# Optimization experiments

Measured on AMD Instinct MI355X. Metric: run time of the kernel, lower is better.

Reference implementation:

```python
import jax, jax.numpy as jnp
import numpy as np

# Mamba dims: d_model=1024, expand=2 -> d_inner=2048, d_state=16, d_conv=4, dt_rank=ceil(1024/16)=64
B, L, D = 2, 1024, 1024
DIN, N, R, K = 2048, 16, 64, 4
LN_EPS = 1e-5


def setup_inputs():
    key = jax.random.key(0)
    ks = jax.random.split(key, 12)
    s = lambda fan_in: 1.0 / np.sqrt(fan_in)
    inp = {
        "x": jax.random.normal(ks[0], (B, L, D), jnp.float32),
        "W_in": jax.random.normal(ks[1], (D, 2 * DIN), jnp.float32) * s(D),
        "conv_w": jax.random.normal(ks[2], (DIN, K), jnp.float32) * s(K),
        "conv_b": jax.random.normal(ks[3], (DIN,), jnp.float32) * 0.02,
        "W_x": jax.random.normal(ks[4], (DIN, R + 2 * N), jnp.float32) * s(DIN),
        "W_dt": jax.random.normal(ks[5], (R, DIN), jnp.float32) * s(R),
        # bias chosen so softplus(bias) ~ small positive dt
        "b_dt": jnp.full((DIN,), -4.0, jnp.float32)
        + jax.random.normal(ks[6], (DIN,), jnp.float32) * 0.1,
        # S4D-real init: A = -[1..N] broadcast over channels
        "A_log": jnp.log(jnp.broadcast_to(jnp.arange(1, N + 1, dtype=jnp.float32), (DIN, N))),
        "D_skip": jnp.ones((DIN,), jnp.float32),
        "W_out": jax.random.normal(ks[7], (DIN, D), jnp.float32) * s(DIN),
        "ln_g": jnp.ones((D,), jnp.float32),
        "ln_b": jnp.zeros((D,), jnp.float32),
    }
    return inp


def _silu(x):
    return x * jax.nn.sigmoid(x)


def _mamba_forward(x, W_in, conv_w, conv_b, W_x, W_dt, b_dt, A_log, D_skip, W_out, ln_g, ln_b):
    # in_proj -> (x_in, z), each [B, L, DIN]
    xz = jnp.einsum("bld,de->ble", x, W_in)
    x_in, z = jnp.split(xz, 2, axis=-1)

    # causal depthwise conv1d (kernel K=4) via shifted sums
    xp = jnp.pad(x_in, ((0, 0), (K - 1, 0), (0, 0)))  # [B, L+K-1, DIN]
    x_conv = conv_b
    for k in range(K):
        x_conv = x_conv + xp[:, k : k + L, :] * conv_w[:, k]
    x_conv = _silu(x_conv)  # [B, L, DIN]

    # x_proj -> dt_rank + 2*N
    x_dbl = jnp.einsum("bld,de->ble", x_conv, W_x)
    dt, Bc, Cc = jnp.split(x_dbl, [R, R + N], axis=-1)  # [B,L,R], [B,L,N], [B,L,N]
    delta = jax.nn.softplus(jnp.einsum("blr,rd->bld", dt, W_dt) + b_dt)  # [B,L,DIN]

    A = -jnp.exp(A_log)  # [DIN, N]
    # discretize: deltaA [B,L,DIN,N], deltaB_u [B,L,DIN,N]
    deltaA = jnp.exp(delta[..., None] * A)
    deltaBu = delta[..., None] * Bc[:, :, None, :] * x_conv[..., None]

    # selective scan over time
    def step(h, inp):
        dA, dBu, C_t = inp  # [B,DIN,N], [B,DIN,N], [B,N]
        h = dA * h + dBu
        y_t = jnp.einsum("bdn,bn->bd", h, C_t)
        return h, y_t

    h0 = jnp.zeros((B, DIN, N), jnp.float32)
    xs = (
        jnp.moveaxis(deltaA, 1, 0),
        jnp.moveaxis(deltaBu, 1, 0),
        jnp.moveaxis(Cc, 1, 0),
    )
    _, ys = jax.lax.scan(step, h0, xs)  # ys: [L, B, DIN]
    y = jnp.moveaxis(ys, 0, 1) + x_conv * D_skip  # [B, L, DIN]

    y = y * _silu(z)
    out = jnp.einsum("bld,de->ble", y, W_out)  # [B, L, D]

    # post LayerNorm
    mu = jnp.mean(out, axis=-1, keepdims=True)
    var = jnp.mean(jnp.square(out - mu), axis=-1, keepdims=True)
    return (out - mu) * jax.lax.rsqrt(var + LN_EPS) * ln_g + ln_b


def reference(x, W_in, conv_w, conv_b, W_x, W_dt, b_dt, A_log, D_skip, W_out, ln_g, ln_b):
    return _mamba_forward(x, W_in, conv_w, conv_b, W_x, W_dt, b_dt, A_log, D_skip, W_out, ln_g, ln_b)
```

## Files before the change

kernel.cpp:

```cpp
#include <hip/hip_runtime.h>

#define LSEQ 1024
#define DMODEL 1024
#define DINNER 2048
#define NSTATE 16
#define RRANK 64
#define CHUNK 32
#define NCHUNK 32
#define KSPLIT 8

typedef unsigned short u16;
typedef __attribute__((ext_vector_type(8))) short bf16x8;
typedef __attribute__((ext_vector_type(4))) float f32x4;

__device__ __forceinline__ float sigmoidf_(float x) {
    return 1.0f / (1.0f + __expf(-x));
}
__device__ __forceinline__ float softplusf_(float x) {
    return (x > 20.0f) ? x : log1pf(__expf(x));
}
__device__ __forceinline__ short f2bf(float f) {
    union { float f; unsigned u; } v; v.f = f;
    unsigned r = v.u + 0x7FFF + ((v.u >> 16) & 1);
    return (short)(r >> 16);
}

__global__ __launch_bounds__(256) void cast_bf16_kernel(
    const float* __restrict__ in, u16* __restrict__ out)
{
    const size_t i = ((size_t)blockIdx.x * 256 + threadIdx.x) * 8;
    float4 a = *(const float4*)&in[i];
    float4 b = *(const float4*)&in[i + 4];
    bf16x8 o;
    o[0] = f2bf(a.x); o[1] = f2bf(a.y); o[2] = f2bf(a.z); o[3] = f2bf(a.w);
    o[4] = f2bf(b.x); o[5] = f2bf(b.y); o[6] = f2bf(b.z); o[7] = f2bf(b.w);
    *(bf16x8*)&out[i] = o;
}

__global__ __launch_bounds__(256) void transpose_cast_kernel(
    const float* __restrict__ in, u16* __restrict__ out, int R, int C)
{
    __shared__ float t[32][33];
    const int bx = blockIdx.x * 32;
    const int by = blockIdx.y * 32;
    const int tx = threadIdx.x % 32, ty = threadIdx.x / 32;
    #pragma unroll
    for (int i = 0; i < 4; ++i)
        t[ty + 8 * i][tx] = in[(size_t)(by + ty + 8 * i) * C + bx + tx];
    __syncthreads();
    #pragma unroll
    for (int i = 0; i < 4; ++i)
        out[(size_t)(bx + ty + 8 * i) * R + by + tx] = (u16)f2bf(t[tx][ty + 8 * i]);
}

template<int BM, int BN>
__global__ __launch_bounds__(256) void mfma_gemm_kernel(
    const u16* __restrict__ A, const u16* __restrict__ Bt,
    float* __restrict__ C0, float* __restrict__ C1,
    int M, int N, int K, int Nsplit)
{
    constexpr int WMS = BM / 32;
    constexpr int WNS = BN / 32;
    __shared__ u16 lA[BM * 32];
    __shared__ u16 lB[BN * 32];

    const int tid  = threadIdx.x;
    const int lane = tid & 63, wave = tid >> 6;
    const int quad = lane >> 4, l16 = lane & 15;
    const int wm   = (wave >> 1) * (BM / 2);
    const int wn   = (wave & 1) * (BN / 2);
    const int row0 = blockIdx.y * BM;
    const int col0 = blockIdx.x * BN;

    float* Cp; int ccol, ldc;
    if (col0 < Nsplit) { Cp = C0; ccol = col0;          ldc = Nsplit; }
    else               { Cp = C1; ccol = col0 - Nsplit; ldc = N - Nsplit; }

    f32x4 acc[WMS][WNS];
    #pragma unroll
    for (int i = 0; i < WMS; ++i)
        #pragma unroll
        for (int j = 0; j < WNS; ++j)
            acc[i][j] = (f32x4){0.f, 0.f, 0.f, 0.f};

    for (int k0 = 0; k0 < K; k0 += 32) {
        #pragma unroll
        for (int t = 0; t < BM / 64; ++t) {
            int c = tid + t * 256;
            int r = c >> 2, kc = c & 3;
            *(bf16x8*)&lA[r * 32 + kc * 8] =
                *(const bf16x8*)&A[(size_t)(row0 + r) * K + k0 + kc * 8];
        }
        #pragma unroll
        for (int t = 0; t < BN / 64; ++t) {
            int c = tid + t * 256;
            int r = c >> 2, kc = c & 3;
            *(bf16x8*)&lB[r * 32 + kc * 8] =
                *(const bf16x8*)&Bt[(size_t)(col0 + r) * K + k0 + kc * 8];
        }
        __syncthreads();
        bf16x8 af[WMS], bfr[WNS];
        #pragma unroll
        for (int i = 0; i < WMS; ++i)
            af[i] = *(bf16x8*)&lA[(wm + i * 16 + l16) * 32 + quad * 8];
        #pragma unroll
        for (int j = 0; j < WNS; ++j)
            bfr[j] = *(bf16x8*)&lB[(wn + j * 16 + l16) * 32 + quad * 8];
        #pragma unroll
        for (int i = 0; i < WMS; ++i)
            #pragma unroll
            for (int j = 0; j < WNS; ++j)
                acc[i][j] = __builtin_amdgcn_mfma_f32_16x16x32_bf16(
                    af[i], bfr[j], acc[i][j], 0, 0, 0);
        __syncthreads();
    }
    #pragma unroll
    for (int i = 0; i < WMS; ++i)
        #pragma unroll
        for (int j = 0; j < WNS; ++j)
            #pragma unroll
            for (int r = 0; r < 4; ++r)
                Cp[(size_t)(row0 + wm + i * 16 + quad * 4 + r) * ldc
                   + ccol + wn + j * 16 + l16] = acc[i][j][r];
}

__global__ __launch_bounds__(256) void conv_silu_kernel(
    const float* __restrict__ X1, const float* __restrict__ cw,
    const float* __restrict__ cb, float* __restrict__ xconv)
{
    const int idx = blockIdx.x * 256 + threadIdx.x;
    const int dq  = idx % (DINNER / 4);
    const int bl  = idx / (DINNER / 4);
    const int l   = bl % LSEQ;
    const int d0  = dq * 4;

    const float4* cw4 = (const float4*)cw;
    const float4 W0 = cw4[d0 + 0];
    const float4 W1 = cw4[d0 + 1];
    const float4 W2 = cw4[d0 + 2];
    const float4 W3 = cw4[d0 + 3];
    float4 s = *(const float4*)&cb[d0];

    #pragma unroll
    for (int k = 0; k < 4; ++k) {
        int ls = l + k - 3;
        if (ls >= 0) {
            float4 xv = *(const float4*)&X1[(size_t)(bl + k - 3) * DINNER + d0];
            s.x = fmaf(xv.x, ((const float*)&W0)[k], s.x);
            s.y = fmaf(xv.y, ((const float*)&W1)[k], s.y);
            s.z = fmaf(xv.z, ((const float*)&W2)[k], s.z);
            s.w = fmaf(xv.w, ((const float*)&W3)[k], s.w);
        }
    }
    s.x *= sigmoidf_(s.x);
    s.y *= sigmoidf_(s.y);
    s.z *= sigmoidf_(s.z);
    s.w *= sigmoidf_(s.w);
    *(float4*)&xconv[(size_t)idx * 4] = s;
}

__global__ __launch_bounds__(256) void xproj_part_kernel(
    const float* __restrict__ xc, const float* __restrict__ Wx,
    float* __restrict__ part)
{
    __shared__ float As[32][64 + 4];
    __shared__ float Ws[32][96 + 4];

    const int tid  = threadIdx.x;
    const int tx   = tid % 32;
    const int ty   = tid / 32;
    const int row0 = blockIdx.x * 64;
    const int k0   = blockIdx.y * (DINNER / KSPLIT);

    float acc[8][3];
    #pragma unroll
    for (int i = 0; i < 8; ++i) { acc[i][0] = 0.f; acc[i][1] = 0.f; acc[i][2] = 0.f; }

    for (int kt = 0; kt < DINNER / KSPLIT; kt += 32) {
        const int kb = k0 + kt;
        #pragma unroll
        for (int i = 0; i < 2; ++i) {
            int lin = tid + i * 256;
            int m = lin / 8, kq = lin % 8;
            float4 v = *(const float4*)&xc[(size_t)(row0 + m) * DINNER + kb + kq * 4];
            As[kq * 4 + 0][m] = v.x;
            As[kq * 4 + 1][m] = v.y;
            As[kq * 4 + 2][m] = v.z;
            As[kq * 4 + 3][m] = v.w;
        }
        #pragma unroll
        for (int i = 0; i < 3; ++i) {
            int lin = tid + i * 256;
            int kk = lin / 24, q = lin % 24;
            *(float4*)&Ws[kk][q * 4] = *(const float4*)&Wx[(size_t)(kb + kk) * 96 + q * 4];
        }
        __syncthreads();
        #pragma unroll 8
        for (int kk = 0; kk < 32; ++kk) {
            float a[8];
            *(float4*)&a[0] = *(const float4*)&As[kk][ty * 8];
            *(float4*)&a[4] = *(const float4*)&As[kk][ty * 8 + 4];
            float b0 = Ws[kk][tx], b1 = Ws[kk][tx + 32], b2 = Ws[kk][tx + 64];
            #pragma unroll
            for (int i = 0; i < 8; ++i) {
                acc[i][0] = fmaf(a[i], b0, acc[i][0]);
                acc[i][1] = fmaf(a[i], b1, acc[i][1]);
                acc[i][2] = fmaf(a[i], b2, acc[i][2]);
            }
        }
        __syncthreads();
    }
    float* po = part + (size_t)blockIdx.y * (2 * LSEQ * 96);
    #pragma unroll
    for (int i = 0; i < 8; ++i) {
        int r = row0 + ty * 8 + i;
        po[(size_t)r * 96 + tx]      = acc[i][0];
        po[(size_t)r * 96 + tx + 32] = acc[i][1];
        po[(size_t)r * 96 + tx + 64] = acc[i][2];
    }
}

__global__ __launch_bounds__(256) void xproj_reduce_kernel(
    const float* __restrict__ part, float* __restrict__ xdbl)
{
    const int idx = blockIdx.x * 256 + threadIdx.x;
    float s = 0.0f;
    #pragma unroll
    for (int k = 0; k < KSPLIT; ++k)
        s += part[(size_t)k * (2 * LSEQ * 96) + idx];
    xdbl[idx] = s;
}

__global__ __launch_bounds__(256) void delta_kernel(
    const float* __restrict__ xdbl, const float* __restrict__ Wdt,
    const float* __restrict__ bdt, float* __restrict__ delta)
{
    __shared__ float As[64][64 + 4];
    __shared__ float Ws[64][64 + 4];
    const int tid  = threadIdx.x;
    const int tx   = tid % 16;
    const int ty   = tid / 16;
    const int row0 = blockIdx.y * 64;
    const int col0 = blockIdx.x * 64;

    #pragma unroll
    for (int i = 0; i < 4; ++i) {
        int lin = tid + i * 256;
        int m = lin / 16, kq = lin % 16;
        float4 v = *(const float4*)&xdbl[(size_t)(row0 + m) * 96 + kq * 4];
        As[kq * 4 + 0][m] = v.x;
        As[kq * 4 + 1][m] = v.y;
        As[kq * 4 + 2][m] = v.z;
        As[kq * 4 + 3][m] = v.w;
    }
    #pragma unroll
    for (int i = 0; i < 4; ++i) {
        int lin = tid + i * 256;
        int kk = lin / 16, q = lin % 16;
        *(float4*)&Ws[kk][q * 4] = *(const float4*)&Wdt[(size_t)kk * DINNER + col0 + q * 4];
    }
    __syncthreads();

    float acc[4][4];
    #pragma unroll
    for (int i = 0; i < 4; ++i)
        #pragma unroll
        for (int j = 0; j < 4; ++j) acc[i][j] = 0.0f;

    #pragma unroll 8
    for (int kk = 0; kk < 64; ++kk) {
        float4 a = *(const float4*)&As[kk][ty * 4];
        float4 b = *(const float4*)&Ws[kk][tx * 4];
        const float* ap = (const float*)&a;
        const float* bp = (const float*)&b;
        #pragma unroll
        for (int i = 0; i < 4; ++i)
            #pragma unroll
            for (int j = 0; j < 4; ++j)
                acc[i][j] = fmaf(ap[i], bp[j], acc[i][j]);
    }

    float4 bv = *(const float4*)&bdt[col0 + tx * 4];
    const float* bvp = (const float*)&bv;
    #pragma unroll
    for (int i = 0; i < 4; ++i) {
        float4 o;
        o.x = softplusf_(acc[i][0] + bvp[0]);
        o.y = softplusf_(acc[i][1] + bvp[1]);
        o.z = softplusf_(acc[i][2] + bvp[2]);
        o.w = softplusf_(acc[i][3] + bvp[3]);
        *(float4*)&delta[(size_t)(row0 + ty * 4 + i) * DINNER + col0 + tx * 4] = o;
    }
}

__global__ __launch_bounds__(256) void scan_part1_kernel(
    const float* __restrict__ delta, const float* __restrict__ xconv,
    const float* __restrict__ xdbl, const float* __restrict__ A_log,
    float* __restrict__ Pbuf, float* __restrict__ Hbuf)
{
    const int d  = blockIdx.x * 256 + threadIdx.x;
    const int b  = blockIdx.y;
    const int ch = blockIdx.z;

    float Aa[NSTATE];
    #pragma unroll
    for (int q = 0; q < 4; ++q) {
        float4 v = *(const float4*)&A_log[(size_t)d * NSTATE + q * 4];
        Aa[q * 4 + 0] = -__expf(v.x);
        Aa[q * 4 + 1] = -__expf(v.y);
        Aa[q * 4 + 2] = -__expf(v.z);
        Aa[q * 4 + 3] = -__expf(v.w);
    }
    float h[NSTATE], P[NSTATE];
    #pragma unroll
    for (int n = 0; n < NSTATE; ++n) { h[n] = 0.0f; P[n] = 1.0f; }

    const size_t row0 = (size_t)b * LSEQ + (size_t)ch * CHUNK;
    #pragma unroll 4
    for (int t = 0; t < CHUNK; ++t) {
        const size_t row = row0 + t;
        float dv  = delta[row * DINNER + d];
        float xcv = xconv[row * DINNER + d];
        float du  = dv * xcv;
        const float4* br = (const float4*)&xdbl[row * 96 + RRANK];
        float4 B4[4] = { br[0], br[1], br[2], br[3] };
        const float* Bv = (const float*)B4;
        #pragma unroll
        for (int n = 0; n < NSTATE; ++n) {
            float dA = __expf(dv * Aa[n]);
            h[n] = fmaf(dA, h[n], du * Bv[n]);
            P[n] *= dA;
        }
    }
    float* Pp = &Pbuf[(((size_t)ch * 2 + b) * DINNER + d) * NSTATE];
    float* Hp = &Hbuf[(((size_t)ch * 2 + b) * DINNER + d) * NSTATE];
    #pragma unroll
    for (int q = 0; q < 4; ++q) {
        *(float4*)&Pp[q * 4] = *(float4*)&P[q * 4];
        *(float4*)&Hp[q * 4] = *(float4*)&h[q * 4];
    }
}

__global__ __launch_bounds__(256) void scan_combine_kernel(
    const float* __restrict__ Pbuf, const float* __restrict__ Hbuf,
    float* __restrict__ h0buf)
{
    const int idx = blockIdx.x * 256 + threadIdx.x;
    float H = 0.0f;
    #pragma unroll 8
    for (int cch = 0; cch < NCHUNK; ++cch) {
        const size_t g = (size_t)cch * (2 * DINNER * NSTATE) + idx;
        h0buf[g] = H;
        H = fmaf(Pbuf[g], H, Hbuf[g]);
    }
}

__global__ __launch_bounds__(256) void scan_part2_kernel(
    const float* __restrict__ delta, const float* __restrict__ xconv,
    const float* __restrict__ xdbl, const float* __restrict__ h0buf,
    const float* __restrict__ Z, u16* __restrict__ yb,
    const float* __restrict__ A_log, const float* __restrict__ Dskip)
{
    const int d  = blockIdx.x * 256 + threadIdx.x;
    const int b  = blockIdx.y;
    const int ch = blockIdx.z;

    float Aa[NSTATE];
    #pragma unroll
    for (int q = 0; q < 4; ++q) {
        float4 v = *(const float4*)&A_log[(size_t)d * NSTATE + q * 4];
        Aa[q * 4 + 0] = -__expf(v.x);
        Aa[q * 4 + 1] = -__expf(v.y);
        Aa[q * 4 + 2] = -__expf(v.z);
        Aa[q * 4 + 3] = -__expf(v.w);
    }
    const float Dd = Dskip[d];

    float h[NSTATE];
    const float* Hp = &h0buf[(((size_t)ch * 2 + b) * DINNER + d) * NSTATE];
    #pragma unroll
    for (int q = 0; q < 4; ++q)
        *(float4*)&h[q * 4] = *(const float4*)&Hp[q * 4];

    const size_t row0 = (size_t)b * LSEQ + (size_t)ch * CHUNK;
    #pragma unroll 2
    for (int t = 0; t < CHUNK; ++t) {
        const size_t row = row0 + t;
        float dv  = delta[row * DINNER + d];
        float xcv = xconv[row * DINNER + d];
        float du  = dv * xcv;
        const float4* br = (const float4*)&xdbl[row * 96 + RRANK];
        float4 BC[8] = { br[0], br[1], br[2], br[3], br[4], br[5], br[6], br[7] };
        const float* Bv = (const float*)BC;
        const float* Cv = Bv + NSTATE;
        float y = 0.0f;
        #pragma unroll
        for (int n = 0; n < NSTATE; ++n) {
            float dA = __expf(dv * Aa[n]);
            h[n] = fmaf(dA, h[n], du * Bv[n]);
            y = fmaf(h[n], Cv[n], y);
        }
        float zz = Z[row * DINNER + d];
        float yv = (y + xcv * Dd) * (zz * sigmoidf_(zz));
        yb[row * DINNER + d] = (u16)f2bf(yv);
    }
}

__global__ __launch_bounds__(256) void ln_kernel(
    const float* __restrict__ t, const float* __restrict__ g,
    const float* __restrict__ b, float* __restrict__ out)
{
    const int row = blockIdx.x;
    const int tid = threadIdx.x;
    float4 v = *(const float4*)&t[(size_t)row * DMODEL + tid * 4];
    float s = v.x + v.y + v.z + v.w;
    float q = v.x * v.x + v.y * v.y + v.z * v.z + v.w * v.w;
    #pragma unroll
    for (int m = 1; m < 64; m <<= 1) {
        s += __shfl_xor(s, m, 64);
        q += __shfl_xor(q, m, 64);
    }
    __shared__ float ss[4], qq[4];
    if ((tid & 63) == 0) { ss[tid >> 6] = s; qq[tid >> 6] = q; }
    __syncthreads();
    float S = ss[0] + ss[1] + ss[2] + ss[3];
    float Q = qq[0] + qq[1] + qq[2] + qq[3];
    float mu  = S * (1.0f / DMODEL);
    float var = Q * (1.0f / DMODEL) - mu * mu;
    float rs  = rsqrtf(var + 1e-5f);
    float4 gv = *(const float4*)&g[tid * 4];
    float4 bv = *(const float4*)&b[tid * 4];
    float4 o;
    o.x = (v.x - mu) * rs * gv.x + bv.x;
    o.y = (v.y - mu) * rs * gv.y + bv.y;
    o.z = (v.z - mu) * rs * gv.z + bv.z;
    o.w = (v.w - mu) * rs * gv.w + bv.w;
    *(float4*)&out[(size_t)row * DMODEL + tid * 4] = o;
}

extern "C" void kernel_launch(void* const* d_in, const int* in_sizes, int n_in,
                              void* d_out, int out_size, void* d_ws, size_t ws_size,
                              hipStream_t stream) {
    const float* x      = (const float*)d_in[0];
    const float* W_in   = (const float*)d_in[1];
    const float* conv_w = (const float*)d_in[2];
    const float* conv_b = (const float*)d_in[3];
    const float* W_x    = (const float*)d_in[4];
    const float* W_dt   = (const float*)d_in[5];
    const float* b_dt   = (const float*)d_in[6];
    const float* A_log  = (const float*)d_in[7];
    const float* D_skip = (const float*)d_in[8];
    const float* W_out  = (const float*)d_in[9];
    const float* ln_g   = (const float*)d_in[10];
    const float* ln_b   = (const float*)d_in[11];
    (void)in_sizes; (void)n_in; (void)out_size; (void)ws_size;

    const int M = 2 * LSEQ;

    float* ws    = (float*)d_ws;
    float* X1    = ws;
    float* Z     = X1    + (size_t)M * DINNER;
    float* xconv = Z     + (size_t)M * DINNER;
    float* xdbl  = xconv + (size_t)M * DINNER;
    float* delta = xdbl  + (size_t)M * 96;
    float* tmp   = delta + (size_t)M * DINNER;
    u16*   xb    = (u16*)(tmp + (size_t)M * DMODEL);
    u16*   Wbin  = xb    + (size_t)M * DMODEL;
    u16*   Wbout = Wbin  + (size_t)2 * DINNER * DMODEL;
    u16*   yb    = (u16*)X1;
    float* Pbuf  = X1 + (size_t)2 * 1024 * 1024;
    float* Hbuf  = (float*)Wbin;
    float* part  = tmp;
    float* h0    = tmp;

    cast_bf16_kernel<<<(M * DMODEL) / (256 * 8), 256, 0, stream>>>(x, xb);
    transpose_cast_kernel<<<dim3((2 * DINNER) / 32, DMODEL / 32), 256, 0, stream>>>(
        W_in, Wbin, DMODEL, 2 * DINNER);
    transpose_cast_kernel<<<dim3(DMODEL / 32, DINNER / 32), 256, 0, stream>>>(
        W_out, Wbout, DINNER, DMODEL);

    mfma_gemm_kernel<128, 128>
        <<<dim3((2 * DINNER) / 128, M / 128), 256, 0, stream>>>(
            xb, Wbin, X1, Z, M, 2 * DINNER, DMODEL, DINNER);

    conv_silu_kernel<<<(M * (DINNER / 4)) / 256, 256, 0, stream>>>(
        X1, conv_w, conv_b, xconv);

    xproj_part_kernel<<<dim3(M / 64, KSPLIT), 256, 0, stream>>>(xconv, W_x, part);
    xproj_reduce_kernel<<<(M * 96) / 256, 256, 0, stream>>>(part, xdbl);

    delta_kernel<<<dim3(DINNER / 64, M / 64), 256, 0, stream>>>(
        xdbl, W_dt, b_dt, delta);

    scan_part1_kernel<<<dim3(DINNER / 256, 2, NCHUNK), 256, 0, stream>>>(
        delta, xconv, xdbl, A_log, Pbuf, Hbuf);
    scan_combine_kernel<<<(2 * DINNER * NSTATE) / 256, 256, 0, stream>>>(
        Pbuf, Hbuf, h0);
    scan_part2_kernel<<<dim3(DINNER / 256, 2, NCHUNK), 256, 0, stream>>>(
        delta, xconv, xdbl, h0, Z, yb, A_log, D_skip);

    mfma_gemm_kernel<64, 64>
        <<<dim3(DMODEL / 64, M / 64), 256, 0, stream>>>(
            yb, Wbout, tmp, tmp, M, DMODEL, DINNER, DMODEL);

    ln_kernel<<<M, 256, 0, stream>>>(tmp, ln_g, ln_b, (float*)d_out);
}
```

Before: 296.4 us.

## Store intermediates in bf16, use async global-to-LDS loads, merge transpose kernels

Z, the conv output, and delta are now written and read as bf16 instead of fp32, which halves the memory traffic of the memory-bound conv, x_proj, and scan kernels. The GEMM loads tiles with global_load_lds direct-to-LDS copies instead of staging through registers, and its split epilogue writes the Z half as bf16. The two weight transpose-cast launches are merged into one. This trades some accuracy in delta and the scan inputs for less bandwidth and fewer launches.

```diff
diff --git a/kernel.cpp b/kernel.cpp
--- a/kernel.cpp
+++ b/kernel.cpp
@@ -11,6 +11,7 @@
 
 typedef unsigned short u16;
 typedef __attribute__((ext_vector_type(8))) short bf16x8;
+typedef __attribute__((ext_vector_type(4))) short bf16x4;
 typedef __attribute__((ext_vector_type(4))) float f32x4;
 
 __device__ __forceinline__ float sigmoidf_(float x) {
@@ -23,6 +24,15 @@
     union { float f; unsigned u; } v; v.f = f;
     unsigned r = v.u + 0x7FFF + ((v.u >> 16) & 1);
     return (short)(r >> 16);
+}
+__device__ __forceinline__ float bf2f(u16 b) {
+    union { unsigned u; float f; } v; v.u = ((unsigned)b) << 16;
+    return v.f;
+}
+__device__ __forceinline__ void async_cp16(const u16* g, u16* l) {
+    __builtin_amdgcn_global_load_lds(
+        (const __attribute__((address_space(1))) unsigned int*)g,
+        (__attribute__((address_space(3))) unsigned int*)l, 16, 0, 0);
 }
 
 __global__ __launch_bounds__(256) void cast_bf16_kernel(
@@ -37,13 +47,17 @@
     *(bf16x8*)&out[i] = o;
 }
 
-__global__ __launch_bounds__(256) void transpose_cast_kernel(
-    const float* __restrict__ in, u16* __restrict__ out, int R, int C)
+__global__ __launch_bounds__(256) void transpose_cast2_kernel(
+    const float* __restrict__ in0, u16* __restrict__ out0,
+    const float* __restrict__ in1, u16* __restrict__ out1)
 {
     __shared__ float t[32][33];
-    const int bx = blockIdx.x * 32;
-    const int by = blockIdx.y * 32;
-    const int tx = threadIdx.x % 32, ty = threadIdx.x / 32;
+    int bid = blockIdx.x;
+    const float* in; u16* out; int R, C, bxi, byi;
+    if (bid < 4096) { in = in0; out = out0; R = DMODEL;  C = 2 * DINNER; bxi = bid & 127; byi = bid >> 7; }
+    else { bid -= 4096; in = in1; out = out1; R = DINNER; C = DMODEL;    bxi = bid & 31;  byi = bid >> 5; }
+    const int bx = bxi * 32, by = byi * 32;
+    const int tx = threadIdx.x & 31, ty = threadIdx.x >> 5;
     #pragma unroll
     for (int i = 0; i < 4; ++i)
         t[ty + 8 * i][tx] = in[(size_t)(by + ty + 8 * i) * C + bx + tx];
@@ -53,10 +67,10 @@
         out[(size_t)(bx + ty + 8 * i) * R + by + tx] = (u16)f2bf(t[tx][ty + 8 * i]);
 }
 
-template<int BM, int BN>
+template<int BM, int BN, bool BSPLIT>
 __global__ __launch_bounds__(256) void mfma_gemm_kernel(
     const u16* __restrict__ A, const u16* __restrict__ Bt,
-    float* __restrict__ C0, float* __restrict__ C1,
+    float* __restrict__ C0, u16* __restrict__ C1,
     int M, int N, int K, int Nsplit)
 {
     constexpr int WMS = BM / 32;
@@ -72,10 +86,6 @@
     const int row0 = blockIdx.y * BM;
     const int col0 = blockIdx.x * BN;
 
-    float* Cp; int ccol, ldc;
-    if (col0 < Nsplit) { Cp = C0; ccol = col0;          ldc = Nsplit; }
-    else               { Cp = C1; ccol = col0 - Nsplit; ldc = N - Nsplit; }
-
     f32x4 acc[WMS][WNS];
     #pragma unroll
     for (int i = 0; i < WMS; ++i)
@@ -88,15 +98,13 @@
         for (int t = 0; t < BM / 64; ++t) {
             int c = tid + t * 256;
             int r = c >> 2, kc = c & 3;
-            *(bf16x8*)&lA[r * 32 + kc * 8] =
-                *(const bf16x8*)&A[(size_t)(row0 + r) * K + k0 + kc * 8];
+            async_cp16(&A[(size_t)(row0 + r) * K + k0 + kc * 8], &lA[c * 8]);
         }
         #pragma unroll
         for (int t = 0; t < BN / 64; ++t) {
             int c = tid + t * 256;
             int r = c >> 2, kc = c & 3;
-            *(bf16x8*)&lB[r * 32 + kc * 8] =
-                *(const bf16x8*)&Bt[(size_t)(col0 + r) * K + k0 + kc * 8];
+            async_cp16(&Bt[(size_t)(col0 + r) * K + k0 + kc * 8], &lB[c * 8]);
         }
         __syncthreads();
         bf16x8 af[WMS], bfr[WNS];
@@ -114,19 +122,32 @@
                     af[i], bfr[j], acc[i][j], 0, 0, 0);
         __syncthreads();
     }
-    #pragma unroll
-    for (int i = 0; i < WMS; ++i)
-        #pragma unroll
-        for (int j = 0; j < WNS; ++j)
+    if (!BSPLIT || col0 < Nsplit) {
+        const int ldc = BSPLIT ? Nsplit : N;
+        #pragma unroll
+        for (int i = 0; i < WMS; ++i)
             #pragma unroll
-            for (int r = 0; r < 4; ++r)
-                Cp[(size_t)(row0 + wm + i * 16 + quad * 4 + r) * ldc
-                   + ccol + wn + j * 16 + l16] = acc[i][j][r];
+            for (int j = 0; j < WNS; ++j)
+                #pragma unroll
+                for (int r = 0; r < 4; ++r)
+                    C0[(size_t)(row0 + wm + i * 16 + quad * 4 + r) * ldc
+                       + col0 + wn + j * 16 + l16] = acc[i][j][r];
+    } else {
+        const int ldc = N - Nsplit, ccol = col0 - Nsplit;
+        #pragma unroll
+        for (int i = 0; i < WMS; ++i)
+            #pragma unroll
+            for (int j = 0; j < WNS; ++j)
+                #pragma unroll
+                for (int r = 0; r < 4; ++r)
+                    C1[(size_t)(row0 + wm + i * 16 + quad * 4 + r) * ldc
+                       + ccol + wn + j * 16 + l16] = (u16)f2bf(acc[i][j][r]);
+    }
 }
 
 __global__ __launch_bounds__(256) void conv_silu_kernel(
     const float* __restrict__ X1, const float* __restrict__ cw,
-    const float* __restrict__ cb, float* __restrict__ xconv)
+    const float* __restrict__ cb, u16* __restrict__ xcb)
 {
     const int idx = blockIdx.x * 256 + threadIdx.x;
     const int dq  = idx % (DINNER / 4);
@@ -152,15 +173,16 @@
             s.w = fmaf(xv.w, ((const float*)&W3)[k], s.w);
         }
     }
-    s.x *= sigmoidf_(s.x);
-    s.y *= sigmoidf_(s.y);
-    s.z *= sigmoidf_(s.z);
-    s.w *= sigmoidf_(s.w);
-    *(float4*)&xconv[(size_t)idx * 4] = s;
+    bf16x4 o;
+    o[0] = f2bf(s.x * sigmoidf_(s.x));
+    o[1] = f2bf(s.y * sigmoidf_(s.y));
+    o[2] = f2bf(s.z * sigmoidf_(s.z));
+    o[3] = f2bf(s.w * sigmoidf_(s.w));
+    *(bf16x4*)&xcb[(size_t)idx * 4] = o;
 }
 
 __global__ __launch_bounds__(256) void xproj_part_kernel(
-    const float* __restrict__ xc, const float* __restrict__ Wx,
+    const u16* __restrict__ xcb, const float* __restrict__ Wx,
     float* __restrict__ part)
 {
     __shared__ float As[32][64 + 4];
@@ -178,15 +200,12 @@
 
     for (int kt = 0; kt < DINNER / KSPLIT; kt += 32) {
         const int kb = k0 + kt;
-        #pragma unroll
-        for (int i = 0; i < 2; ++i) {
-            int lin = tid + i * 256;
-            int m = lin / 8, kq = lin % 8;
-            float4 v = *(const float4*)&xc[(size_t)(row0 + m) * DINNER + kb + kq * 4];
-            As[kq * 4 + 0][m] = v.x;
-            As[kq * 4 + 1][m] = v.y;
-            As[kq * 4 + 2][m] = v.z;
-            As[kq * 4 + 3][m] = v.w;
+        {
+            int m = tid >> 2, kq = tid & 3;
+            bf16x8 v = *(const bf16x8*)&xcb[(size_t)(row0 + m) * DINNER + kb + kq * 8];
+            #pragma unroll
+            for (int j = 0; j < 8; ++j)
+                As[kq * 8 + j][m] = bf2f((u16)v[j]);
         }
         #pragma unroll
         for (int i = 0; i < 3; ++i) {
@@ -233,7 +252,7 @@
 
 __global__ __launch_bounds__(256) void delta_kernel(
     const float* __restrict__ xdbl, const float* __restrict__ Wdt,
-    const float* __restrict__ bdt, float* __restrict__ delta)
+    const float* __restrict__ bdt, u16* __restrict__ deltab)
 {
     __shared__ float As[64][64 + 4];
     __shared__ float Ws[64][64 + 4];
@@ -284,17 +303,17 @@
     const float* bvp = (const float*)&bv;
     #pragma unroll
     for (int i = 0; i < 4; ++i) {
-        float4 o;
-        o.x = softplusf_(acc[i][0] + bvp[0]);
-        o.y = softplusf_(acc[i][1] + bvp[1]);
-        o.z = softplusf_(acc[i][2] + bvp[2]);
-        o.w = softplusf_(acc[i][3] + bvp[3]);
-        *(float4*)&delta[(size_t)(row0 + ty * 4 + i) * DINNER + col0 + tx * 4] = o;
+        bf16x4 o;
+        o[0] = f2bf(softplusf_(acc[i][0] + bvp[0]));
+        o[1] = f2bf(softplusf_(acc[i][1] + bvp[1]));
+        o[2] = f2bf(softplusf_(acc[i][2] + bvp[2]));
+        o[3] = f2bf(softplusf_(acc[i][3] + bvp[3]));
+        *(bf16x4*)&deltab[(size_t)(row0 + ty * 4 + i) * DINNER + col0 + tx * 4] = o;
     }
 }
 
 __global__ __launch_bounds__(256) void scan_part1_kernel(
-    const float* __restrict__ delta, const float* __restrict__ xconv,
+    const u16* __restrict__ deltab, const u16* __restrict__ xcb,
     const float* __restrict__ xdbl, const float* __restrict__ A_log,
     float* __restrict__ Pbuf, float* __restrict__ Hbuf)
 {
@@ -319,8 +338,8 @@
     #pragma unroll 4
     for (int t = 0; t < CHUNK; ++t) {
         const size_t row = row0 + t;
-        float dv  = delta[row * DINNER + d];
-        float xcv = xconv[row * DINNER + d];
+        float dv  = bf2f(deltab[row * DINNER + d]);
+        float xcv = bf2f(xcb[row * DINNER + d]);
         float du  = dv * xcv;
         const float4* br = (const float4*)&xdbl[row * 96 + RRANK];
         float4 B4[4] = { br[0], br[1], br[2], br[3] };
@@ -356,9 +375,9 @@
 }
 
 __global__ __launch_bounds__(256) void scan_part2_kernel(
-    const float* __restrict__ delta, const float* __restrict__ xconv,
+    const u16* __restrict__ deltab, const u16* __restrict__ xcb,
     const float* __restrict__ xdbl, const float* __restrict__ h0buf,
-    const float* __restrict__ Z, u16* __restrict__ yb,
+    const u16* __restrict__ Zb, u16* __restrict__ yb,
     const float* __restrict__ A_log, const float* __restrict__ Dskip)
 {
     const int d  = blockIdx.x * 256 + threadIdx.x;
@@ -386,8 +405,8 @@
     #pragma unroll 2
     for (int t = 0; t < CHUNK; ++t) {
         const size_t row = row0 + t;
-        float dv  = delta[row * DINNER + d];
-        float xcv = xconv[row * DINNER + d];
+        float dv  = bf2f(deltab[row * DINNER + d]);
+        float xcv = bf2f(xcb[row * DINNER + d]);
         float du  = dv * xcv;
         const float4* br = (const float4*)&xdbl[row * 96 + RRANK];
         float4 BC[8] = { br[0], br[1], br[2], br[3], br[4], br[5], br[6], br[7] };
@@ -400,7 +419,7 @@
             h[n] = fmaf(dA, h[n], du * Bv[n]);
             y = fmaf(h[n], Cv[n], y);
         }
-        float zz = Z[row * DINNER + d];
+        float zz = bf2f(Zb[row * DINNER + d]);
         float yv = (y + xcv * Dd) * (zz * sigmoidf_(zz));
         yb[row * DINNER + d] = (u16)f2bf(yv);
     }
@@ -459,49 +478,49 @@
 
     float* ws    = (float*)d_ws;
     float* X1    = ws;
-    float* Z     = X1    + (size_t)M * DINNER;
-    float* xconv = Z     + (size_t)M * DINNER;
-    float* xdbl  = xconv + (size_t)M * DINNER;
-    float* delta = xdbl  + (size_t)M * 96;
-    float* tmp   = delta + (size_t)M * DINNER;
+    float* Zs    = X1    + (size_t)M * DINNER;
+    float* xcs   = Zs    + (size_t)M * DINNER;
+    float* xdbl  = xcs   + (size_t)M * DINNER;
+    float* dls   = xdbl  + (size_t)M * 96;
+    float* tmp   = dls   + (size_t)M * DINNER;
     u16*   xb    = (u16*)(tmp + (size_t)M * DMODEL);
     u16*   Wbin  = xb    + (size_t)M * DMODEL;
     u16*   Wbout = Wbin  + (size_t)2 * DINNER * DMODEL;
-    u16*   yb    = (u16*)X1;
-    float* Pbuf  = X1 + (size_t)2 * 1024 * 1024;
-    float* Hbuf  = (float*)Wbin;
-    float* part  = tmp;
-    float* h0    = tmp;
+    u16*   Zb     = (u16*)Zs;
+    u16*   xcb    = (u16*)xcs;
+    u16*   deltab = (u16*)dls;
+    u16*   yb     = (u16*)X1;
+    float* Pbuf   = X1 + (size_t)2 * 1024 * 1024;
+    float* Hbuf   = (float*)Wbin;
+    float* part   = tmp;
+    float* h0     = tmp;
 
     cast_bf16_kernel<<<(M * DMODEL) / (256 * 8), 256, 0, stream>>>(x, xb);
-    transpose_cast_kernel<<<dim3((2 * DINNER) / 32, DMODEL / 32), 256, 0, stream>>>(
-        W_in, Wbin, DMODEL, 2 * DINNER);
-    transpose_cast_kernel<<<dim3(DMODEL / 32, DINNER / 32), 256, 0, stream>>>(
-        W_out, Wbout, DINNER, DMODEL);
-
-    mfma_gemm_kernel<128, 128>
+    transpose_cast2_kernel<<<4096 + 2048, 256, 0, stream>>>(W_in, Wbin, W_out, Wbout);
+
+    mfma_gemm_kernel<128, 128, true>
         <<<dim3((2 * DINNER) / 128, M / 128), 256, 0, stream>>>(
-            xb, Wbin, X1, Z, M, 2 * DINNER, DMODEL, DINNER);
+            xb, Wbin, X1, Zb, M, 2 * DINNER, DMODEL, DINNER);
 
     conv_silu_kernel<<<(M * (DINNER / 4)) / 256, 256, 0, stream>>>(
-        X1, conv_w, conv_b, xconv);
-
-    xproj_part_kernel<<<dim3(M / 64, KSPLIT), 256, 0, stream>>>(xconv, W_x, part);
+        X1, conv_w, conv_b, xcb);
+
+    xproj_part_kernel<<<dim3(M / 64, KSPLIT), 256, 0, stream>>>(xcb, W_x, part);
     xproj_reduce_kernel<<<(M * 96) / 256, 256, 0, stream>>>(part, xdbl);
 
     delta_kernel<<<dim3(DINNER / 64, M / 64), 256, 0, stream>>>(
-        xdbl, W_dt, b_dt, delta);
+        xdbl, W_dt, b_dt, deltab);
 
     scan_part1_kernel<<<dim3(DINNER / 256, 2, NCHUNK), 256, 0, stream>>>(
-        delta, xconv, xdbl, A_log, Pbuf, Hbuf);
+        deltab, xcb, xdbl, A_log, Pbuf, Hbuf);
     scan_combine_kernel<<<(2 * DINNER * NSTATE) / 256, 256, 0, stream>>>(
         Pbuf, Hbuf, h0);
     scan_part2_kernel<<<dim3(DINNER / 256, 2, NCHUNK), 256, 0, stream>>>(
-        delta, xconv, xdbl, h0, Z, yb, A_log, D_skip);
-
-    mfma_gemm_kernel<64, 64>
+        deltab, xcb, xdbl, h0, Zb, yb, A_log, D_skip);
+
+    mfma_gemm_kernel<64, 64, false>
         <<<dim3(DMODEL / 64, M / 64), 256, 0, stream>>>(
-            yb, Wbout, tmp, tmp, M, DMODEL, DINNER, DMODEL);
+            yb, Wbout, tmp, (u16*)nullptr, M, DMODEL, DINNER, DMODEL);
 
     ln_kernel<<<M, 256, 0, stream>>>(tmp, ln_g, ln_b, (float*)d_out);
 }
```

Result: faster. 277.6 us (-6.3%).
